# Performance work log

Measured on AMD Instinct MI355X. Metric: run time of the kernel, lower is better.

Reference implementation:

```python
import jax, jax.numpy as jnp
import numpy as np

V_PATCH_NUMS = (1, 2, 3, 4, 5, 6, 8, 10, 13, 16)


def _pool_matrix(in_size: int, out_size: int) -> jnp.ndarray:
    # Matrix form of torch adaptive_avg_pool1d (== F.interpolate mode='area'):
    # window i averages input bins [floor(i*in/out), ceil((i+1)*in/out)).
    M = np.zeros((out_size, in_size), dtype=np.float32)
    for i in range(out_size):
        s = (i * in_size) // out_size
        e = -((-(i + 1) * in_size) // out_size)  # ceil division
        M[i, s:e] = 1.0 / (e - s)
    return jnp.asarray(M)


def setup_inputs() -> dict:
    key = jax.random.key(0)
    k1, k2 = jax.random.split(key)
    B, C, H, W = 64, 32, 16, 16
    vocab = 4096
    f = jax.random.normal(k1, (B, C, H, W), dtype=jnp.float32)
    # embedding init: uniform(-1/vocab, 1/vocab), as in the torch module
    emb = (jax.random.uniform(k2, (vocab, C), dtype=jnp.float32) * 2.0 - 1.0) / vocab
    return {"f": f, "emb": emb}


def reference(f, emb):
    # Multi-scale residual VQ: per scale -> area-downsample residual,
    # nearest-codebook argmin, embedding gather, bicubic-upsample,
    # accumulate into f_hat and subtract from f_rest.
    B, C, H, W = f.shape
    f = jax.lax.stop_gradient(f)            # f_no_grad in torch
    x = jnp.transpose(f, (0, 2, 3, 1))      # BHWC for resize/gather
    f_rest = x
    f_hat = jnp.zeros_like(x)
    emb_ng = jax.lax.stop_gradient(emb)     # distances use embedding.weight.data
    e_sq = jnp.sum(emb_ng * emb_ng, axis=1)  # [vocab]
    SN = len(V_PATCH_NUMS)
    for si, pn in enumerate(V_PATCH_NUMS):
        last = si == SN - 1
        if last:
            z = f_rest                       # [B,H,W,C]
        else:
            Mh = _pool_matrix(H, pn)
            Mw = _pool_matrix(W, pn)
            z = jnp.einsum('ph,qw,bhwc->bpqc', Mh, Mw, f_rest)  # area interp
        z_NC = z.reshape(-1, C)
        # squared L2 distance to every code: ||z||^2 + ||e||^2 - 2 z e^T
        d = jnp.sum(z_NC * z_NC, axis=1, keepdims=True) + e_sq - 2.0 * (z_NC @ emb_ng.T)
        idx = jnp.argmin(d, axis=1).reshape(B, pn, pn)
        h = emb[idx]                         # [B,pn,pn,C] gather (grad-carrying emb)
        if not last:
            h = jax.image.resize(h, (B, H, W, C), method='cubic')  # bicubic up
        f_hat = f_hat + h
        f_rest = f_rest - h
    return jnp.transpose(f_hat, (0, 3, 1, 2))  # back to BCHW
```

## Files before the change

### kernel.cpp

```cpp
#include <hip/hip_runtime.h>
#include <math.h>

#define WS_ESQ   0
#define WS_STATE 4096
#define WS_FHAT  (4096 + 524288)
#define WS_Z     (4096 + 2*524288)
#define WS_PSC   (4096 + 3*524288)
#define WS_PIX   (4096 + 3*524288 + 131072)

__device__ __forceinline__ float4 v4add(float4 a, float4 b) {
    return make_float4(__fadd_rn(a.x,b.x), __fadd_rn(a.y,b.y),
                       __fadd_rn(a.z,b.z), __fadd_rn(a.w,b.w));
}
__device__ __forceinline__ float4 v4sq(float4 a) {
    return make_float4(__fmul_rn(a.x,a.x), __fmul_rn(a.y,a.y),
                       __fmul_rn(a.z,a.z), __fmul_rn(a.w,a.w));
}
__device__ __forceinline__ float np_pw32(float4 q0, float4 q1, float4 q2, float4 q3,
                                         float4 q4, float4 q5, float4 q6, float4 q7) {
    float4 rA = v4add(v4add(v4add(q0, q2), q4), q6);
    float4 rB = v4add(v4add(v4add(q1, q3), q5), q7);
    float l = __fadd_rn(__fadd_rn(rA.x, rA.y), __fadd_rn(rA.z, rA.w));
    float h = __fadd_rn(__fadd_rn(rB.x, rB.y), __fadd_rn(rB.z, rB.w));
    return __fadd_rn(l, h);
}

__device__ __forceinline__ double keys64(double x) {
    if (x < 1.0)      return ((1.5*x - 2.5)*x)*x + 1.0;
    else if (x < 2.0) return ((-0.5*x + 2.5)*x - 4.0)*x + 2.0;
    return 0.0;
}

__global__ __launch_bounds__(256) void vq_apply(
    const float* __restrict__ f, const float* __restrict__ emb,
    float* __restrict__ esq, float* __restrict__ state, float* __restrict__ fhat,
    float* __restrict__ zws, const float* __restrict__ psc, const int* __restrict__ pix,
    int sIdx, int pn, int pnPrev, int ncbPrev)
{
    __shared__ float fr[1280];
    __shared__ float hs[676];
    __shared__ int   idx_arr[176];
    __shared__ float U[256];
    __shared__ float red_f[1360];
    __shared__ int   red_i[1360];

    const int tid = threadIdx.x;
    const int wg  = blockIdx.x;
    if (wg >= 512) {
        int j = ((wg - 512) << 8) + tid;
        const float4* e4 = (const float4*)(emb + (size_t)j*32);
        esq[j] = np_pw32(v4sq(e4[0]),v4sq(e4[1]),v4sq(e4[2]),v4sq(e4[3]),
                         v4sq(e4[4]),v4sq(e4[5]),v4sq(e4[6]),v4sq(e4[7]));
        return;
    }
    const int b  = wg >> 3;
    const int c0 = (wg & 7) * 4;

    const float* src = (sIdx <= 1) ? f : state;
    for (int o = tid; o < 1024; o += 256) {
        int cc = o >> 8, yx = o & 255;
        fr[yx*5 + cc] = src[b*8192 + (c0 + cc)*256 + yx];
    }
    __syncthreads();

    if (sIdx > 0) {
        const int Vp = pnPrev * pnPrev;
        const int step = ncbPrev >> 3;
        for (int t = tid; t < Vp*8; t += 256) {
            int v = t >> 3, k = t & 7;
            const size_t base = (size_t)((v << 6) + b) * ncbPrev;
            float best = INFINITY; int bi = 0;
            for (int ch = k*step; ch < (k+1)*step; ++ch) {
                float sc = psc[base + ch];
                if (sc < best) { best = sc; bi = pix[base + ch]; }
            }
            red_f[t] = best; red_i[t] = bi;
        }
        __syncthreads();
        if (tid < Vp) {
            float best = INFINITY; int bi = 0;
            for (int k = 0; k < 8; ++k) {
                float sc = red_f[tid*8 + k];
                if (sc < best) { best = sc; bi = red_i[tid*8 + k]; }
            }
            idx_arr[tid] = bi;
        }
        __syncthreads();
        for (int t = tid; t < Vp*4; t += 256)
            hs[t] = emb[(size_t)idx_arr[t >> 2]*32 + c0 + (t & 3)];
        if (tid < 16) {
            double scl = 16.0 / (double)pnPrev;
            double inv = 1.0 / scl;
            double sp = ((double)tid + 0.5) * inv - 0.5;
            double w64[16]; double tot = 0.0;
            for (int q = 0; q < pnPrev; ++q) {
                double wv = keys64(fabs(sp - (double)q));
                w64[q] = wv; tot += wv;
            }
            for (int q = 0; q < pnPrev; ++q) U[tid*16 + q] = (float)(w64[q] / tot);
        }
        __syncthreads();
        {
            const double inv = 1.0 / (16.0 / (double)pnPrev);
            const int yx = tid, y = yx >> 4, x = yx & 15;
            double sy = ((double)y + 0.5) * inv - 0.5;
            double sx = ((double)x + 0.5) * inv - 0.5;
            int p0 = (int)floor(sy) - 1, q0 = (int)floor(sx) - 1;
            int pa = max(0, p0), pb = min(pnPrev - 1, p0 + 3);
            int qa = max(0, q0), qb = min(pnPrev - 1, q0 + 3);
            float acc0 = 0.f, acc1 = 0.f, acc2 = 0.f, acc3 = 0.f;
            for (int p = pa; p <= pb; ++p) {
                float wy = U[y*16 + p];
                for (int q = qa; q <= qb; ++q) {
                    float wx = U[x*16 + q];
                    const float* hp = &hs[(p*pnPrev + q)*4];
                    acc0 = __fadd_rn(acc0, __fmul_rn(__fmul_rn(hp[0], wy), wx));
                    acc1 = __fadd_rn(acc1, __fmul_rn(__fmul_rn(hp[1], wy), wx));
                    acc2 = __fadd_rn(acc2, __fmul_rn(__fmul_rn(hp[2], wy), wx));
                    acc3 = __fadd_rn(acc3, __fmul_rn(__fmul_rn(hp[3], wy), wx));
                }
            }
            float a4[4] = {acc0, acc1, acc2, acc3};
            #pragma unroll
            for (int cc = 0; cc < 4; ++cc) {
                float frv = __fsub_rn(fr[yx*5 + cc], a4[cc]);
                fr[yx*5 + cc] = frv;
                int go = b*8192 + (c0 + cc)*256 + yx;
                state[go] = frv;
                fhat[go] = (sIdx == 1) ? a4[cc] : __fadd_rn(fhat[go], a4[cc]);
            }
        }
        __syncthreads();
    }

    const int V = pn * pn;
    if (pn < 16) {
        if (tid < V) {
            int p = tid / pn, q = tid - p*pn;
            int sh = (p*16)/pn, eh = ((p+1)*16 + pn - 1)/pn;
            int sw = (q*16)/pn, ew = ((q+1)*16 + pn - 1)/pn;
            float Mh = (float)(1.0/(double)(eh - sh));
            float Mw = (float)(1.0/(double)(ew - sw));
            float coef = __fmul_rn(Mh, Mw);
            float a4[4] = {0.f, 0.f, 0.f, 0.f};
            for (int hh = sh; hh < eh; ++hh)
                for (int wy = sw; wy < ew; ++wy) {
                    const float* fp = &fr[(hh*16 + wy)*5];
                    #pragma unroll
                    for (int cc = 0; cc < 4; ++cc)
                        a4[cc] = __fadd_rn(a4[cc], __fmul_rn(coef, fp[cc]));
                }
            *(float4*)(zws + (size_t)((tid << 6) + b)*32 + c0) =
                make_float4(a4[0], a4[1], a4[2], a4[3]);
        }
    } else {
        const int yx = tid;
        *(float4*)(zws + (size_t)((yx << 6) + b)*32 + c0) =
            make_float4(fr[yx*5], fr[yx*5 + 1], fr[yx*5 + 2], fr[yx*5 + 3]);
    }
}

#define DOT4P(EP, K, ZA, ZB) { float4 ev = EP[K]; \
    acc0 = __fmaf_rn(ev.x, ZA.x, acc0); acc1 = __fmaf_rn(ev.x, ZB.x, acc1); \
    acc0 = __fmaf_rn(ev.y, ZA.y, acc0); acc1 = __fmaf_rn(ev.y, ZB.y, acc1); \
    acc0 = __fmaf_rn(ev.z, ZA.z, acc0); acc1 = __fmaf_rn(ev.z, ZB.z, acc1); \
    acc0 = __fmaf_rn(ev.w, ZA.w, acc0); acc1 = __fmaf_rn(ev.w, ZB.w, acc1); }

__global__ __launch_bounds__(256, 4) void vq_scan(
    const float* __restrict__ emb, const float* __restrict__ esq,
    const float* __restrict__ zws, float* __restrict__ psc, int* __restrict__ pix,
    int V, int ncbMask, int ncbShift, int CB)
{
    __shared__ float ebuf[2][2048];
    __shared__ float esq_l[512];
    __shared__ float red_f[512];
    __shared__ int   red_i[512];

    const int tid  = threadIdx.x;
    const int cb   = blockIdx.x & ncbMask;
    const int pblk = blockIdx.x >> ncbShift;
    const int w    = tid >> 6, lane = tid & 63;
    const int N    = V << 6;

    const int pair0 = (pblk << 7) + lane;
    const int p0c = min(pair0, N - 1), p1c = min(pair0 + 64, N - 1);
    const float4* za = (const float4*)(zws + (size_t)p0c*32);
    const float4* zb = (const float4*)(zws + (size_t)p1c*32);
    float4 a0 = za[0], a1 = za[1], a2 = za[2], a3 = za[3];
    float4 a4 = za[4], a5 = za[5], a6 = za[6], a7 = za[7];
    float4 b0 = zb[0], b1 = zb[1], b2 = zb[2], b3 = zb[3];
    float4 b4 = zb[4], b5 = zb[5], b6 = zb[6], b7 = zb[7];
    float zsq0 = np_pw32(v4sq(a0),v4sq(a1),v4sq(a2),v4sq(a3),
                         v4sq(a4),v4sq(a5),v4sq(a6),v4sq(a7));
    float zsq1 = np_pw32(v4sq(b0),v4sq(b1),v4sq(b2),v4sq(b3),
                         v4sq(b4),v4sq(b5),v4sq(b6),v4sq(b7));

    const int jchunk = cb * CB;
    for (int t = tid; t < CB; t += 256) esq_l[t] = esq[jchunk + t];

    const int tsz   = (CB < 64) ? CB : 64;
    const int ntile = CB / tsz;
    const int wsl   = tsz >> 2;
    const int nf4   = tsz << 3;

    {
        const float4* g = (const float4*)(emb + (size_t)jchunk*32);
        for (int t = tid; t < nf4; t += 256) ((float4*)ebuf[0])[t] = g[t];
    }
    __syncthreads();

    float best0 = INFINITY, best1 = INFINITY; int bi0 = 0, bi1 = 0;
    for (int tile = 0; tile < ntile; ++tile) {
        const int cur = tile & 1;
        if (tile + 1 < ntile) {
            const float4* g = (const float4*)(emb + (size_t)(jchunk + (tile+1)*tsz)*32);
            for (int t = tid; t < nf4; t += 256) ((float4*)ebuf[cur ^ 1])[t] = g[t];
        }
        const float* eb = ebuf[cur];
        const int lbase = w * wsl;
        for (int i = 0; i < wsl; ++i) {
            const int lc = lbase + i;
            const float4* e4 = (const float4*)(eb + lc*32);
            float acc0 = 0.f, acc1 = 0.f;
            DOT4P(e4, 0, a0, b0) DOT4P(e4, 1, a1, b1) DOT4P(e4, 2, a2, b2) DOT4P(e4, 3, a3, b3)
            DOT4P(e4, 4, a4, b4) DOT4P(e4, 5, a5, b5) DOT4P(e4, 6, a6, b6) DOT4P(e4, 7, a7, b7)
            float sqj = esq_l[tile*tsz + lc];
            float d0 = __fsub_rn(__fadd_rn(zsq0, sqj), __fmul_rn(2.0f, acc0));
            float d1 = __fsub_rn(__fadd_rn(zsq1, sqj), __fmul_rn(2.0f, acc1));
            int j = jchunk + tile*tsz + lc;
            if (d0 < best0) { best0 = d0; bi0 = j; }
            if (d1 < best1) { best1 = d1; bi1 = j; }
        }
        __syncthreads();
    }
    red_f[w*128 + lane]      = best0;  red_i[w*128 + lane]      = bi0;
    red_f[w*128 + 64 + lane] = best1;  red_i[w*128 + 64 + lane] = bi1;
    __syncthreads();

    if (tid < 128) {
        const int p = (pblk << 7) + tid;
        if (p < N) {
            float bb = INFINITY; int bi = 0x7fffffff;
            #pragma unroll
            for (int ww = 0; ww < 4; ++ww) {
                float sc = red_f[ww*128 + tid];
                int   ji = red_i[ww*128 + tid];
                if (sc < bb || (sc == bb && ji < bi)) { bb = sc; bi = ji; }
            }
            psc[(size_t)p*(ncbMask + 1) + cb] = bb;
            pix[(size_t)p*(ncbMask + 1) + cb] = bi;
        }
    }
}

__global__ __launch_bounds__(256) void vq_final(
    const float* __restrict__ emb, const float* __restrict__ fhat,
    const float* __restrict__ psc, const int* __restrict__ pix,
    float* __restrict__ out)
{
    __shared__ int idx_arr[256];
    const int tid = threadIdx.x;
    const int b = blockIdx.x;
    {
        float best = INFINITY; int bi = 0;
        const size_t pb0 = (size_t)((tid << 6) + b) * 8;
        for (int ch = 0; ch < 8; ++ch) {
            float sc = psc[pb0 + ch];
            if (sc < best) { best = sc; bi = pix[pb0 + ch]; }
        }
        idx_arr[tid] = bi;
    }
    __syncthreads();
    for (int o = tid; o < 8192; o += 256) {
        int c = o >> 8, yx = o & 255;
        out[b*8192 + o] = __fadd_rn(fhat[(size_t)b*8192 + o],
                                    emb[(size_t)idx_arr[yx]*32 + c]);
    }
}

extern "C" void kernel_launch(void* const* d_in, const int* in_sizes, int n_in,
                              void* d_out, int out_size, void* d_ws, size_t ws_size,
                              hipStream_t stream) {
    const float* f   = (const float*)d_in[0];
    const float* emb = (const float*)d_in[1];
    float* ws  = (float*)d_ws;
    float* out = (float*)d_out;
    float* esq   = ws + WS_ESQ;
    float* state = ws + WS_STATE;
    float* fhatp = ws + WS_FHAT;
    float* zws   = ws + WS_Z;
    float* psc   = ws + WS_PSC;
    int*   pixp  = (int*)(ws + WS_PIX);
    static const int pns[10]  = {1, 2, 3, 4, 5, 6, 8, 10, 13, 16};
    static const int ncbl[10] = {7, 7, 6, 6, 5, 5, 4, 4, 3, 3};

    for (int s = 0; s < 10; ++s) {
        int pn = pns[s], V = pn*pn, sh = ncbl[s];
        int PB = ((V << 6) + 127) >> 7;
        vq_apply<<<(s == 0) ? 528 : 512, 256, 0, stream>>>(
            f, emb, esq, state, fhatp, zws, psc, pixp,
            s, pn, s > 0 ? pns[s-1] : 0, s > 0 ? (1 << ncbl[s-1]) : 0);
        vq_scan<<<PB << sh, 256, 0, stream>>>(emb, esq, zws, psc, pixp,
                                              V, (1 << sh) - 1, sh, 4096 >> sh);
    }
    vq_final<<<64, 256, 0, stream>>>(emb, fhatp, psc, pixp, out);
}
```

Before: 430.0 us.

## Stream codebook rows via scalar loads instead of LDS double-buffered tiles

Replaces the shared-memory double-buffered codebook tiles with per-wave scalar (SMEM) loads of each code vector and its squared norm. Each wave scans a contiguous quarter of the chunk and loads each code's 32 floats into SGPRs, which the FMAs use directly as wave-uniform operands. This removes the LDS traffic and the per-tile barriers. In exchange, every code waits on a blocking s_waitcnt with no prefetch, so scalar-load latency is exposed once per code.

```diff
diff --git a/kernel.cpp b/kernel.cpp
--- a/kernel.cpp
+++ b/kernel.cpp
@@ -160,19 +160,39 @@
     }
 }
 
-#define DOT4P(EP, K, ZA, ZB) { float4 ev = EP[K]; \
-    acc0 = __fmaf_rn(ev.x, ZA.x, acc0); acc1 = __fmaf_rn(ev.x, ZB.x, acc1); \
-    acc0 = __fmaf_rn(ev.y, ZA.y, acc0); acc1 = __fmaf_rn(ev.y, ZB.y, acc1); \
-    acc0 = __fmaf_rn(ev.z, ZA.z, acc0); acc1 = __fmaf_rn(ev.z, ZB.z, acc1); \
-    acc0 = __fmaf_rn(ev.w, ZA.w, acc0); acc1 = __fmaf_rn(ev.w, ZB.w, acc1); }
+typedef float f32x16 __attribute__((ext_vector_type(16)));
+
+#define SLOADW(E0, E1, SQ, JS) { \
+    const float* _pe = emb + ((size_t)(JS) << 5); \
+    const float* _pq = esq + (JS); \
+    asm volatile("s_load_dwordx16 %0, %3, 0x0\n\t" \
+                 "s_load_dwordx16 %1, %3, 0x40\n\t" \
+                 "s_load_dword    %2, %4, 0x0\n\t" \
+                 "s_waitcnt lgkmcnt(0)" \
+        : "=&s"(E0), "=&s"(E1), "=&s"(SQ) : "s"(_pe), "s"(_pq)); }
+
+#define DOT4S(EV, K, ZA, ZB) { \
+    const float ex_ = EV[4*(K)+0], ey_ = EV[4*(K)+1]; \
+    const float ez_ = EV[4*(K)+2], ew_ = EV[4*(K)+3]; \
+    acc0 = __fmaf_rn(ex_, ZA.x, acc0); acc1 = __fmaf_rn(ex_, ZB.x, acc1); \
+    acc0 = __fmaf_rn(ey_, ZA.y, acc0); acc1 = __fmaf_rn(ey_, ZB.y, acc1); \
+    acc0 = __fmaf_rn(ez_, ZA.z, acc0); acc1 = __fmaf_rn(ez_, ZB.z, acc1); \
+    acc0 = __fmaf_rn(ew_, ZA.w, acc0); acc1 = __fmaf_rn(ew_, ZB.w, acc1); }
+
+#define CODE_STEP(E0, E1, SQ, J) { \
+    float acc0 = 0.f, acc1 = 0.f; \
+    DOT4S(E0, 0, a0, b0) DOT4S(E0, 1, a1, b1) DOT4S(E0, 2, a2, b2) DOT4S(E0, 3, a3, b3) \
+    DOT4S(E1, 0, a4, b4) DOT4S(E1, 1, a5, b5) DOT4S(E1, 2, a6, b6) DOT4S(E1, 3, a7, b7) \
+    float d0 = __fsub_rn(__fadd_rn(zsq0, SQ), __fmul_rn(2.0f, acc0)); \
+    float d1 = __fsub_rn(__fadd_rn(zsq1, SQ), __fmul_rn(2.0f, acc1)); \
+    if (d0 < best0) { best0 = d0; bi0 = (J); } \
+    if (d1 < best1) { best1 = d1; bi1 = (J); } }
 
 __global__ __launch_bounds__(256, 4) void vq_scan(
     const float* __restrict__ emb, const float* __restrict__ esq,
     const float* __restrict__ zws, float* __restrict__ psc, int* __restrict__ pix,
     int V, int ncbMask, int ncbShift, int CB)
 {
-    __shared__ float ebuf[2][2048];
-    __shared__ float esq_l[512];
     __shared__ float red_f[512];
     __shared__ int   red_i[512];
 
@@ -196,43 +216,18 @@
                          v4sq(b4),v4sq(b5),v4sq(b6),v4sq(b7));
 
     const int jchunk = cb * CB;
-    for (int t = tid; t < CB; t += 256) esq_l[t] = esq[jchunk + t];
-
-    const int tsz   = (CB < 64) ? CB : 64;
-    const int ntile = CB / tsz;
-    const int wsl   = tsz >> 2;
-    const int nf4   = tsz << 3;
-
-    {
-        const float4* g = (const float4*)(emb + (size_t)jchunk*32);
-        for (int t = tid; t < nf4; t += 256) ((float4*)ebuf[0])[t] = g[t];
-    }
-    __syncthreads();
+    const int pw     = CB >> 2;
+    const int w_u    = __builtin_amdgcn_readfirstlane(w);
+    const int jbase  = jchunk + w_u * pw;
 
     float best0 = INFINITY, best1 = INFINITY; int bi0 = 0, bi1 = 0;
-    for (int tile = 0; tile < ntile; ++tile) {
-        const int cur = tile & 1;
-        if (tile + 1 < ntile) {
-            const float4* g = (const float4*)(emb + (size_t)(jchunk + (tile+1)*tsz)*32);
-            for (int t = tid; t < nf4; t += 256) ((float4*)ebuf[cur ^ 1])[t] = g[t];
-        }
-        const float* eb = ebuf[cur];
-        const int lbase = w * wsl;
-        for (int i = 0; i < wsl; ++i) {
-            const int lc = lbase + i;
-            const float4* e4 = (const float4*)(eb + lc*32);
-            float acc0 = 0.f, acc1 = 0.f;
-            DOT4P(e4, 0, a0, b0) DOT4P(e4, 1, a1, b1) DOT4P(e4, 2, a2, b2) DOT4P(e4, 3, a3, b3)
-            DOT4P(e4, 4, a4, b4) DOT4P(e4, 5, a5, b5) DOT4P(e4, 6, a6, b6) DOT4P(e4, 7, a7, b7)
-            float sqj = esq_l[tile*tsz + lc];
-            float d0 = __fsub_rn(__fadd_rn(zsq0, sqj), __fmul_rn(2.0f, acc0));
-            float d1 = __fsub_rn(__fadd_rn(zsq1, sqj), __fmul_rn(2.0f, acc1));
-            int j = jchunk + tile*tsz + lc;
-            if (d0 < best0) { best0 = d0; bi0 = j; }
-            if (d1 < best1) { best1 = d1; bi1 = j; }
-        }
-        __syncthreads();
-    }
+    for (int i = 0; i < pw; ++i) {
+        const int j = jbase + i;
+        f32x16 e0, e1; float q;
+        SLOADW(e0, e1, q, j);
+        CODE_STEP(e0, e1, q, j);
+    }
+
     red_f[w*128 + lane]      = best0;  red_i[w*128 + lane]      = bi0;
     red_f[w*128 + 64 + lane] = best1;  red_i[w*128 + 64 + lane] = bi1;
     __syncthreads();
```

Result: faster. 418.6 us (-2.7%).
